# Performance work log

Measured on AMD Instinct MI355X. Metric: run time of the kernel, lower is better.

Reference implementation:

```python
import jax, jax.numpy as jnp
import numpy as np

DIM = 2048
N_HEADS = 16
HEAD_DIM = DIM // N_HEADS
ROPE_DIMS = 16
SEQ_LEN = 512
BATCH = 16


def _rope_cache(T):
    # freqs: [T, rd/2]
    inv = 1.0 / (10000.0 ** (jnp.arange(0, ROPE_DIMS, 2, dtype=jnp.float32) / ROPE_DIMS))
    t = jnp.arange(T, dtype=jnp.float32)
    freqs = jnp.outer(t, inv)
    return jnp.cos(freqs), jnp.sin(freqs)


def _apply_rope(x, cos, sin):
    # x: [B, H, T, hd]; rotate first ROPE_DIMS dims (half-split style)
    rd = ROPE_DIMS
    x_rope, x_pass = x[..., :rd], x[..., rd:]
    x1, x2 = x_rope[..., : rd // 2], x_rope[..., rd // 2:]
    c = cos[None, None, :, :]
    s = sin[None, None, :, :]
    rot = jnp.concatenate([x1 * c - x2 * s, x2 * c + x1 * s], axis=-1)
    return jnp.concatenate([rot, x_pass], axis=-1)


def setup_inputs() -> dict:
    key = jax.random.key(0)
    k1, k2, k3 = jax.random.split(key, 3)
    x = jax.random.normal(k1, (BATCH, SEQ_LEN, DIM), dtype=jnp.float32)
    Wqkv = jax.random.normal(k2, (DIM, 3 * DIM), dtype=jnp.float32) * (1.0 / np.sqrt(DIM))
    Wout = jax.random.normal(k3, (DIM, DIM), dtype=jnp.float32) * (1.0 / np.sqrt(DIM))
    return {"x": x, "Wqkv": Wqkv, "Wout": Wout}


def reference(x, Wqkv, Wout):
    B, T, C = x.shape
    H, hd = N_HEADS, HEAD_DIM
    qkv = (x @ Wqkv).reshape(B, T, 3, H, hd)
    q, k, v = qkv[:, :, 0], qkv[:, :, 1], qkv[:, :, 2]  # [B, T, H, hd]
    q = jnp.transpose(q, (0, 2, 1, 3))  # [B, H, T, hd]
    k = jnp.transpose(k, (0, 2, 1, 3))
    v = jnp.transpose(v, (0, 2, 1, 3))
    cos, sin = _rope_cache(T)
    q = _apply_rope(q, cos, sin)
    k = _apply_rope(k, cos, sin)
    scale = 1.0 / np.sqrt(hd)
    scores = jnp.einsum('bhqd,bhkd->bhqk', q, k) * scale
    causal = jnp.tril(jnp.ones((T, T), dtype=bool))
    scores = jnp.where(causal[None, None], scores, jnp.finfo(scores.dtype).min)
    attn = jax.nn.softmax(scores, axis=-1)
    y = jnp.einsum('bhqk,bhkd->bhqd', attn, v)  # [B, H, T, hd]
    y = jnp.transpose(y, (0, 2, 1, 3)).reshape(B, T, C)
    return y @ Wout
```

## Files before the change

kernel.cpp:

```cpp
#include <hip/hip_runtime.h>
#include <hip/hip_bf16.h>
#include <math.h>

using bf16 = __hip_bfloat16;
typedef short s16x8 __attribute__((ext_vector_type(8)));
typedef short s16x4 __attribute__((ext_vector_type(4)));
typedef float f32x4 __attribute__((ext_vector_type(4)));

#define DIM_C   2048
#define NHEADS  16
#define HEADD   128
#define SEQT    512
#define NBATCH  16
#define MROWS   (NBATCH*SEQT)
#define QKVN    (3*DIM_C)

static __device__ __forceinline__ float bf2f(bf16 v){ return __bfloat162float(v); }

static __device__ __forceinline__ void gl16(const void* g, void* l){
    __builtin_amdgcn_global_load_lds(
        reinterpret_cast<__attribute__((address_space(1))) void*>(
            (unsigned long long)g),
        reinterpret_cast<__attribute__((address_space(3))) void*>(
            (unsigned long long)l),
        16, 0, 0);
}

__global__ void k_cvt(const float* __restrict__ in, bf16* __restrict__ out, int n){
    size_t i = ((size_t)blockIdx.x*blockDim.x + threadIdx.x)*8;
    if (i >= (size_t)n) return;
    float4 a = *(const float4*)(in+i);
    float4 b = *(const float4*)(in+i+4);
    union { bf16 o[8]; s16x8 v; } u;
    u.o[0]=__float2bfloat16(a.x); u.o[1]=__float2bfloat16(a.y);
    u.o[2]=__float2bfloat16(a.z); u.o[3]=__float2bfloat16(a.w);
    u.o[4]=__float2bfloat16(b.x); u.o[5]=__float2bfloat16(b.y);
    u.o[6]=__float2bfloat16(b.z); u.o[7]=__float2bfloat16(b.w);
    *(s16x8*)(out+i) = u.v;
}

__global__ void k_transpose_cvt(const float* __restrict__ in, bf16* __restrict__ out,
                                int R, int C){
    __shared__ float tile[32][33];
    int c0 = blockIdx.x*32, r0 = blockIdx.y*32;
    int tx = threadIdx.x, ty = threadIdx.y;
    #pragma unroll
    for(int i=0;i<4;i++)
        tile[ty+8*i][tx] = in[(size_t)(r0+ty+8*i)*C + c0+tx];
    __syncthreads();
    #pragma unroll
    for(int i=0;i<4;i++)
        out[(size_t)(c0+ty+8*i)*R + r0+tx] = __float2bfloat16(tile[tx][ty+8*i]);
}

__global__ void k_vtrans(const bf16* __restrict__ qkv, bf16* __restrict__ vt){
    __shared__ bf16 tile[32][33];
    int t0 = blockIdx.x*32, d0 = blockIdx.y*32, bh = blockIdx.z;
    int b = bh>>4, h = bh&15;
    int tx = threadIdx.x, ty = threadIdx.y;
    const bf16* src = qkv + ((size_t)b*SEQT)*QKVN + 2*DIM_C + (size_t)h*HEADD;
    #pragma unroll
    for(int i=0;i<4;i++)
        tile[ty+8*i][tx] = src[(size_t)(t0+ty+8*i)*QKVN + d0+tx];
    __syncthreads();
    bf16* dst = vt + ((size_t)bh*HEADD)*SEQT;
    #pragma unroll
    for(int i=0;i<4;i++)
        dst[(size_t)(d0+ty+8*i)*SEQT + t0+tx] = tile[tx][ty+8*i];
}

__global__ void k_rope(bf16* __restrict__ qkv){
    int tid = blockIdx.x*blockDim.x + threadIdx.x;
    int i   = tid & 7;        int rest = tid >> 3;
    int qk  = rest & 1;       rest >>= 1;
    int h   = rest & 15;      rest >>= 4;
    int t   = rest & 511;     int b = rest >> 9;
    size_t base = ((size_t)(b*SEQT + t))*QKVN + (size_t)qk*DIM_C + (size_t)h*HEADD;
    float x1 = bf2f(qkv[base+i]), x2 = bf2f(qkv[base+i+8]);
    float inv = powf(10000.f, -(float)i/8.f);
    float fr = (float)t * inv;
    float c = cosf(fr), s = sinf(fr);
    qkv[base+i]   = __float2bfloat16(x1*c - x2*s);
    qkv[base+i+8] = __float2bfloat16(x2*c + x1*s);
}

static __device__ __forceinline__ void store_c(bf16* p, float v){ *p = __float2bfloat16(v); }
static __device__ __forceinline__ void store_c(float* p, float v){ *p = v; }

#define BAR()   __builtin_amdgcn_s_barrier()
#define SCHED() __builtin_amdgcn_sched_barrier(0)
#define LGKM0() asm volatile("s_waitcnt lgkmcnt(0)" ::: "memory")
#define VM6()   asm volatile("s_waitcnt vmcnt(6)"   ::: "memory")
#define VM0()   asm volatile("s_waitcnt vmcnt(0)"   ::: "memory")

template<typename OutT>
__global__ __launch_bounds__(512, 2) void k_gemm256(const bf16* __restrict__ A,
                                                    const bf16* __restrict__ Bt,
                                                    OutT* __restrict__ C,
                                                    int M, int N, int K){
    __shared__ __align__(16) bf16 As[2][2][128*64];
    __shared__ __align__(16) bf16 Bs[2][2][128*64];
    const int tid = threadIdx.x;
    const int wave = tid>>6, lane = tid&63, quad = lane>>4, l16 = lane&15;
    const int wm = wave>>2, wn = wave&3;

    const int nbx = gridDim.x;
    const int nwg = gridDim.x*gridDim.y;
    int bid = blockIdx.y*nbx + blockIdx.x;
    int swz = (bid&7)*(nwg>>3) + (bid>>3);
    int by = swz / nbx, bx = swz - by*nbx;
    const size_t rowbase = (size_t)by * 256;
    const size_t colbase = (size_t)bx * 256;
    const int NT = K>>6;

    f32x4 acc[8][4];
    #pragma unroll
    for(int i=0;i<8;i++)
        #pragma unroll
        for(int j=0;j<4;j++) acc[i][j] = (f32x4)(0.f);

    auto stageA = [&](int kt, int mh, bf16* dst){
        #pragma unroll
        for(int i=0;i<2;i++){
            int cb = i*512 + wave*64;
            int cc = cb + lane;
            int ri = cc>>3;
            int g  = (cc&7) ^ (ri&7);
            size_t grow = rowbase + (size_t)((ri>>6)<<7) + (mh<<6) + (ri&63);
            gl16(A + grow*(size_t)K + kt + g*8, dst + cb*8);
        }
    };
    auto stageB = [&](int kt, int nh, bf16* dst){
        #pragma unroll
        for(int i=0;i<2;i++){
            int cb = i*512 + wave*64;
            int cc = cb + lane;
            int ri = cc>>3;
            int g  = (cc&7) ^ (ri&7);
            size_t grow = colbase + (size_t)((ri>>5)<<6) + (nh<<5) + (ri&31);
            gl16(Bt + grow*(size_t)K + kt + g*8, dst + cb*8);
        }
    };
    auto ldsA = [&](int buf, int mh, int mi, int kc)->s16x8{
        int ri = wm*64 + mi*16 + l16;
        return *(const s16x8*)(&As[buf][mh][ri*64 + (((kc*4+quad) ^ (ri&7))<<3)]);
    };
    auto ldsB = [&](int buf, int nh, int nj, int kc)->s16x8{
        int ri = wn*32 + nj*16 + l16;
        return *(const s16x8*)(&Bs[buf][nh][ri*64 + (((kc*4+quad) ^ (ri&7))<<3)]);
    };

    s16x8 af[4][2], bf0[2][2], bf1[2][2];

#define MFMA16(MH,NH,BFR)                                                        \
    do{ _Pragma("unroll")                                                        \
        for(int mi_=0;mi_<4;mi_++){ _Pragma("unroll")                            \
            for(int nj_=0;nj_<2;nj_++){ _Pragma("unroll")                        \
                for(int kc_=0;kc_<2;kc_++)                                       \
                    acc[(MH)*4+mi_][(NH)*2+nj_] =                                \
                        __builtin_amdgcn_mfma_f32_16x16x32_bf16(                 \
                            af[mi_][kc_], BFR[nj_][kc_],                         \
                            acc[(MH)*4+mi_][(NH)*2+nj_], 0,0,0); } } }while(0)

    stageA(0, 0, &As[0][0][0]);
    stageB(0, 0, &Bs[0][0][0]);
    stageB(0, 1, &Bs[0][1][0]);
    stageA(0, 1, &As[0][1][0]);
    stageA(64, 0, &As[1][0][0]);
    stageB(64, 0, &Bs[1][0][0]);
    stageB(64, 1, &Bs[1][1][0]);
    VM6();
    BAR(); SCHED();

    for(int g=0; g<NT; ++g){
        const int cur = g&1, nxt = cur^1;
        const int kt1 = (g+1)<<6, kt2 = (g+2)<<6;
        #pragma unroll
        for(int mi=0;mi<4;mi++){ af[mi][0]=ldsA(cur,0,mi,0); af[mi][1]=ldsA(cur,0,mi,1); }
        #pragma unroll
        for(int nj=0;nj<2;nj++){ bf0[nj][0]=ldsB(cur,0,nj,0); bf0[nj][1]=ldsB(cur,0,nj,1); }
        if (g+1 < NT) stageA(kt1, 1, &As[nxt][1][0]);
        BAR(); LGKM0(); SCHED();
        __builtin_amdgcn_s_setprio(1);
        MFMA16(0,0,bf0);
        __builtin_amdgcn_s_setprio(0);
        BAR(); SCHED();
        #pragma unroll
        for(int nj=0;nj<2;nj++){ bf1[nj][0]=ldsB(cur,1,nj,0); bf1[nj][1]=ldsB(cur,1,nj,1); }
        if (g+2 < NT) stageA(kt2, 0, &As[cur][0][0]);
        BAR(); LGKM0(); SCHED();
        __builtin_amdgcn_s_setprio(1);
        MFMA16(0,1,bf1);
        __builtin_amdgcn_s_setprio(0);
        BAR(); SCHED();
        #pragma unroll
        for(int mi=0;mi<4;mi++){ af[mi][0]=ldsA(cur,1,mi,0); af[mi][1]=ldsA(cur,1,mi,1); }
        if (g+2 < NT) stageB(kt2, 0, &Bs[cur][0][0]);
        BAR(); LGKM0(); SCHED();
        __builtin_amdgcn_s_setprio(1);
        MFMA16(1,0,bf0);
        __builtin_amdgcn_s_setprio(0);
        BAR(); SCHED();
        if (g+2 < NT){ stageB(kt2, 1, &Bs[cur][1][0]); VM6(); } else { VM0(); }
        BAR(); SCHED();
        __builtin_amdgcn_s_setprio(1);
        MFMA16(1,1,bf1);
        __builtin_amdgcn_s_setprio(0);
        BAR(); SCHED();
    }
#undef MFMA16

    #pragma unroll
    for(int mf=0;mf<8;mf++)
        #pragma unroll
        for(int nf=0;nf<4;nf++)
            #pragma unroll
            for(int r=0;r<4;r++){
                size_t row = rowbase + wm*128 + mf*16 + quad*4 + r;
                size_t col = colbase + wn*64  + nf*16 + l16;
                store_c(C + row*(size_t)N + col, acc[mf][nf][r]);
            }
}

__global__ __launch_bounds__(256, 4) void k_attn(const bf16* __restrict__ qkv,
                                                 const bf16* __restrict__ vt,
                                                 bf16* __restrict__ y){
    __shared__ __align__(16) bf16 Ks[64*128];
    __shared__ __align__(16) bf16 Vs[128*64];
    __shared__ __align__(16) bf16 Ps[64*64];
    const int id = blockIdx.x;
    const int x  = id & 7, g = id >> 3;
    const int qt = 7 - (g >> 5);
    const int bh = ((g & 31) << 3) | x;
    const int b = bh >> 4, h = bh & 15;
    const int tid = threadIdx.x, wave = tid>>6, lane = tid&63, quad = lane>>4, l16 = lane&15;
    const int qbase = qt*64;
    const size_t rs = QKVN;
    const bf16* Qg = qkv + ((size_t)b*SEQT)*rs + (size_t)h*HEADD;
    const bf16* Kg = Qg + DIM_C;
    const bf16* Vtbh = vt + ((size_t)bh*HEADD)*SEQT;

    s16x8 qf[4];
    const int qrow = qbase + wave*16 + l16;
    {
        #pragma unroll
        for(int kc=0;kc<4;kc++)
            qf[kc] = *(const s16x8*)(Qg + (size_t)qrow*rs + kc*32 + quad*8);
    }
    f32x4 acc_o[8];
    #pragma unroll
    for(int dt=0;dt<8;dt++) acc_o[dt] = (f32x4)(0.f);
    float lsum = 0.f;
    const float C2 = 0.12751745f;
    const int nkt = qt + 1;

    for(int kt=0; kt<nkt; kt++){
        const int kbase = kt*64;
        const bool diag = (kt == nkt-1);
        __syncthreads();
        #pragma unroll
        for(int i=0;i<4;i++){
            int base = wave*256 + i*64;
            int cc   = base + lane;
            int rk   = cc>>4, gk = (cc&15) ^ (rk&7);
            gl16(Kg + (size_t)(kbase+rk)*rs + gk*8, &Ks[base*8]);
            int rv   = cc>>3, gv = (cc&7) ^ (rv&7);
            gl16(Vtbh + (size_t)rv*SEQT + kbase + gv*8, &Vs[base*8]);
        }
        __syncthreads();
        f32x4 sacc[4];
        #pragma unroll
        for(int ni=0;ni<4;ni++) sacc[ni] = (f32x4)(0.f);
        #pragma unroll
        for(int kc=0;kc<4;kc++){
            const int ch = kc*4 + quad;
            #pragma unroll
            for(int ni=0;ni<4;ni++){
                int r = ni*16 + l16;
                s16x8 kf = *(const s16x8*)(&Ks[r*128 + ((ch ^ (r&7))*8)]);
                sacc[ni] = __builtin_amdgcn_mfma_f32_16x16x32_bf16(kf, qf[kc], sacc[ni], 0,0,0);
            }
        }
        {
            const int row = wave*16 + l16;
            const int r7  = row & 7;
            #pragma unroll
            for(int ni=0;ni<4;ni++){
                union { s16x4 v; bf16 hh[4]; } pk;
                #pragma unroll
                for(int rr=0;rr<4;rr++){
                    float e = exp2f(sacc[ni][rr]*C2);
                    if (diag){ int kcol = kbase + ni*16 + quad*4 + rr; if (kcol > qrow) e = 0.f; }
                    lsum += e;
                    pk.hh[rr] = __float2bfloat16(e);
                }
                int c = ni*2 + (quad>>1);
                *(s16x4*)(&Ps[row*64 + ((c ^ r7)<<3) + ((quad&1)<<2)]) = pk.v;
            }
        }
        #pragma unroll
        for(int kk=0;kk<2;kk++){
            int rw = wave*16 + l16;
            int c  = kk*4 + quad;
            s16x8 pf = *(const s16x8*)(&Ps[rw*64 + ((c ^ (rw&7))<<3)]);
            #pragma unroll
            for(int dt=0;dt<8;dt++){
                int r = dt*16 + l16;
                s16x8 vf = *(const s16x8*)(&Vs[r*64 + ((c ^ (r&7))<<3)]);
                acc_o[dt] = __builtin_amdgcn_mfma_f32_16x16x32_bf16(vf, pf, acc_o[dt], 0,0,0);
            }
        }
    }
    lsum += __shfl_xor(lsum, 16, 64);
    lsum += __shfl_xor(lsum, 32, 64);
    float inv_l = 1.f/lsum;
    size_t base = ((size_t)(b*SEQT) + qrow)*DIM_C + (size_t)h*HEADD;
    #pragma unroll
    for(int dt=0;dt<8;dt++){
        union { s16x4 v; bf16 hh[4]; } o;
        #pragma unroll
        for(int rr=0;rr<4;rr++) o.hh[rr] = __float2bfloat16(acc_o[dt][rr]*inv_l);
        *(s16x4*)(y + base + dt*16 + quad*4) = o.v;
    }
}

extern "C" void kernel_launch(void* const* d_in, const int* in_sizes, int n_in,
                              void* d_out, int out_size, void* d_ws, size_t ws_size,
                              hipStream_t stream){
    const float* x    = (const float*)d_in[0];
    const float* Wqkv = (const float*)d_in[1];
    const float* Wout = (const float*)d_in[2];
    float* out = (float*)d_out;
    char* ws = (char*)d_ws;
    bf16* xb    = (bf16*)(ws + 0);
    bf16* vt    = (bf16*)(ws + 0);
    bf16* wqkvT = (bf16*)(ws + 33554432);
    bf16* woutT = (bf16*)(ws + 58720256);
    bf16* qkv   = (bf16*)(ws + 67108864);
    bf16* yb    = (bf16*)(ws + 167772160);

    k_cvt<<<dim3(MROWS*DIM_C/8/256), 256, 0, stream>>>(x, xb, MROWS*DIM_C);
    dim3 tb(32,8);
    k_transpose_cvt<<<dim3(QKVN/32, DIM_C/32), tb, 0, stream>>>(Wqkv, wqkvT, DIM_C, QKVN);
    k_transpose_cvt<<<dim3(DIM_C/32, DIM_C/32), tb, 0, stream>>>(Wout, woutT, DIM_C, DIM_C);

    k_gemm256<bf16><<<dim3(QKVN/256, MROWS/256), 512, 0, stream>>>(xb, wqkvT, qkv, MROWS, QKVN, DIM_C);
    k_rope<<<dim3(NBATCH*SEQT*NHEADS*2*8/256), 256, 0, stream>>>(qkv);
    k_vtrans<<<dim3(SEQT/32, HEADD/32, NBATCH*NHEADS), tb, 0, stream>>>(qkv, vt);
    k_attn<<<dim3(SEQT/64 * NHEADS * NBATCH), 256, 0, stream>>>(qkv, vt, yb);
    k_gemm256<float><<<dim3(DIM_C/256, MROWS/256), 512, 0, stream>>>(yb, woutT, out, MROWS, DIM_C, DIM_C);
}
```

Measured before the change: 509.1 us.

## Prefetch LDS fragments ahead of MFMA blocks in the GEMM main loop

Restructures the 256-tile GEMM loop so LDS fragment reads for the next MFMA block (and for the next k-tile) are issued before or during the current MFMA group, instead of being read and then fully waited on with lgkmcnt(0). This hides LDS latency behind matrix work. The MFMA loop order is also changed to kc-outer. The explicit lgkmcnt waits are removed and the compiler is left to insert the dependency waits. This risks more register pressure and relies on barrier placement to keep the double-buffered LDS reads correct.

```diff
diff --git a/kernel.cpp b/kernel.cpp
--- a/kernel.cpp
+++ b/kernel.cpp
@@ -89,7 +89,6 @@
 
 #define BAR()   __builtin_amdgcn_s_barrier()
 #define SCHED() __builtin_amdgcn_sched_barrier(0)
-#define LGKM0() asm volatile("s_waitcnt lgkmcnt(0)" ::: "memory")
 #define VM6()   asm volatile("s_waitcnt vmcnt(6)"   ::: "memory")
 #define VM0()   asm volatile("s_waitcnt vmcnt(0)"   ::: "memory")
 
@@ -152,11 +151,30 @@
 
     s16x8 af[4][2], bf0[2][2], bf1[2][2];
 
+    auto readA = [&](int buf, int mh){
+        #pragma unroll
+        for(int kc=0;kc<2;kc++)
+            #pragma unroll
+            for(int mi=0;mi<4;mi++) af[mi][kc] = ldsA(buf, mh, mi, kc);
+    };
+    auto readB0 = [&](int buf){
+        #pragma unroll
+        for(int kc=0;kc<2;kc++)
+            #pragma unroll
+            for(int nj=0;nj<2;nj++) bf0[nj][kc] = ldsB(buf, 0, nj, kc);
+    };
+    auto readB1 = [&](int buf){
+        #pragma unroll
+        for(int kc=0;kc<2;kc++)
+            #pragma unroll
+            for(int nj=0;nj<2;nj++) bf1[nj][kc] = ldsB(buf, 1, nj, kc);
+    };
+
 #define MFMA16(MH,NH,BFR)                                                        \
     do{ _Pragma("unroll")                                                        \
-        for(int mi_=0;mi_<4;mi_++){ _Pragma("unroll")                            \
-            for(int nj_=0;nj_<2;nj_++){ _Pragma("unroll")                        \
-                for(int kc_=0;kc_<2;kc_++)                                       \
+        for(int kc_=0;kc_<2;kc_++){ _Pragma("unroll")                            \
+            for(int mi_=0;mi_<4;mi_++){ _Pragma("unroll")                        \
+                for(int nj_=0;nj_<2;nj_++)                                       \
                     acc[(MH)*4+mi_][(NH)*2+nj_] =                                \
                         __builtin_amdgcn_mfma_f32_16x16x32_bf16(                 \
                             af[mi_][kc_], BFR[nj_][kc_],                         \
@@ -171,42 +189,41 @@
     stageB(64, 1, &Bs[1][1][0]);
     VM6();
     BAR(); SCHED();
+    readB0(0);
+    readA(0, 0);
 
     for(int g=0; g<NT; ++g){
         const int cur = g&1, nxt = cur^1;
         const int kt1 = (g+1)<<6, kt2 = (g+2)<<6;
-        #pragma unroll
-        for(int mi=0;mi<4;mi++){ af[mi][0]=ldsA(cur,0,mi,0); af[mi][1]=ldsA(cur,0,mi,1); }
-        #pragma unroll
-        for(int nj=0;nj<2;nj++){ bf0[nj][0]=ldsB(cur,0,nj,0); bf0[nj][1]=ldsB(cur,0,nj,1); }
+        readB1(cur);
         if (g+1 < NT) stageA(kt1, 1, &As[nxt][1][0]);
-        BAR(); LGKM0(); SCHED();
+        SCHED(); BAR(); SCHED();
         __builtin_amdgcn_s_setprio(1);
         MFMA16(0,0,bf0);
         __builtin_amdgcn_s_setprio(0);
-        BAR(); SCHED();
-        #pragma unroll
-        for(int nj=0;nj<2;nj++){ bf1[nj][0]=ldsB(cur,1,nj,0); bf1[nj][1]=ldsB(cur,1,nj,1); }
+        SCHED(); BAR();
         if (g+2 < NT) stageA(kt2, 0, &As[cur][0][0]);
-        BAR(); LGKM0(); SCHED();
+        SCHED(); BAR(); SCHED();
         __builtin_amdgcn_s_setprio(1);
         MFMA16(0,1,bf1);
         __builtin_amdgcn_s_setprio(0);
-        BAR(); SCHED();
-        #pragma unroll
-        for(int mi=0;mi<4;mi++){ af[mi][0]=ldsA(cur,1,mi,0); af[mi][1]=ldsA(cur,1,mi,1); }
+        readA(cur, 1);
+        SCHED(); BAR();
         if (g+2 < NT) stageB(kt2, 0, &Bs[cur][0][0]);
-        BAR(); LGKM0(); SCHED();
+        SCHED(); BAR(); SCHED();
         __builtin_amdgcn_s_setprio(1);
         MFMA16(1,0,bf0);
         __builtin_amdgcn_s_setprio(0);
-        BAR(); SCHED();
+        SCHED(); BAR();
         if (g+2 < NT){ stageB(kt2, 1, &Bs[cur][1][0]); VM6(); } else { VM0(); }
-        BAR(); SCHED();
+        SCHED(); BAR(); SCHED();
+        if (g+1 < NT) readB0(nxt);
+        SCHED();
         __builtin_amdgcn_s_setprio(1);
         MFMA16(1,1,bf1);
         __builtin_amdgcn_s_setprio(0);
-        BAR(); SCHED();
+        if (g+1 < NT) readA(nxt, 0);
+        SCHED(); BAR();
     }
 #undef MFMA16
 
```

After: 507.7 us. No clear change (-0.3%).

## Load A fragments directly from global to registers, stage only B via LDS

Applied to the files above, without the earlier changes.

The GEMM stops staging the A tile through shared memory and has each wave load its A fragments straight from global memory into registers. Only B goes through the double-buffered LDS pipeline, and the wait counts and barrier schedule are reworked around the new loads. This halves LDS use and removes the A LDS writes and reads, which could raise occupancy and cut LDS traffic. In exchange, the A loads are issued per wave without cross-wave reuse and their global latency sits close to the MFMAs, so stalls become more likely.

```diff
diff --git a/kernel.cpp b/kernel.cpp
--- a/kernel.cpp
+++ b/kernel.cpp
@@ -89,8 +89,7 @@
 
 #define BAR()   __builtin_amdgcn_s_barrier()
 #define SCHED() __builtin_amdgcn_sched_barrier(0)
-#define LGKM0() asm volatile("s_waitcnt lgkmcnt(0)" ::: "memory")
-#define VM6()   asm volatile("s_waitcnt vmcnt(6)"   ::: "memory")
+#define VM4()   asm volatile("s_waitcnt vmcnt(4)"   ::: "memory")
 #define VM0()   asm volatile("s_waitcnt vmcnt(0)"   ::: "memory")
 
 template<typename OutT>
@@ -98,7 +97,6 @@
                                                     const bf16* __restrict__ Bt,
                                                     OutT* __restrict__ C,
                                                     int M, int N, int K){
-    __shared__ __align__(16) bf16 As[2][2][128*64];
     __shared__ __align__(16) bf16 Bs[2][2][128*64];
     const int tid = threadIdx.x;
     const int wave = tid>>6, lane = tid&63, quad = lane>>4, l16 = lane&15;
@@ -119,17 +117,6 @@
         #pragma unroll
         for(int j=0;j<4;j++) acc[i][j] = (f32x4)(0.f);
 
-    auto stageA = [&](int kt, int mh, bf16* dst){
-        #pragma unroll
-        for(int i=0;i<2;i++){
-            int cb = i*512 + wave*64;
-            int cc = cb + lane;
-            int ri = cc>>3;
-            int g  = (cc&7) ^ (ri&7);
-            size_t grow = rowbase + (size_t)((ri>>6)<<7) + (mh<<6) + (ri&63);
-            gl16(A + grow*(size_t)K + kt + g*8, dst + cb*8);
-        }
-    };
     auto stageB = [&](int kt, int nh, bf16* dst){
         #pragma unroll
         for(int i=0;i<2;i++){
@@ -141,74 +128,83 @@
             gl16(Bt + grow*(size_t)K + kt + g*8, dst + cb*8);
         }
     };
-    auto ldsA = [&](int buf, int mh, int mi, int kc)->s16x8{
-        int ri = wm*64 + mi*16 + l16;
-        return *(const s16x8*)(&As[buf][mh][ri*64 + (((kc*4+quad) ^ (ri&7))<<3)]);
-    };
     auto ldsB = [&](int buf, int nh, int nj, int kc)->s16x8{
         int ri = wn*32 + nj*16 + l16;
         return *(const s16x8*)(&Bs[buf][nh][ri*64 + (((kc*4+quad) ^ (ri&7))<<3)]);
     };
 
+    const bf16* aRow[4];
+    #pragma unroll
+    for(int mi=0;mi<4;mi++)
+        aRow[mi] = A + (rowbase + (size_t)(wm*128 + mi*16 + l16))*(size_t)K + quad*8;
+    const size_t mhK = (size_t)64*(size_t)K;
+
     s16x8 af[4][2], bf0[2][2], bf1[2][2];
 
-#define MFMA16(MH,NH,BFR)                                                        \
-    do{ _Pragma("unroll")                                                        \
+#define LOAD_A(MH, KT) do{ _Pragma("unroll")                                     \
+    for(int mi_=0;mi_<4;mi_++){ _Pragma("unroll")                                \
+        for(int kc_=0;kc_<2;kc_++)                                               \
+            af[mi_][kc_] = *(const s16x8*)(aRow[mi_] + ((MH)?mhK:0)              \
+                                           + (size_t)(KT) + kc_*32); } }while(0)
+#define READ_B0(buf) do{ _Pragma("unroll")                                       \
+    for(int kc_=0;kc_<2;kc_++){ _Pragma("unroll")                                \
+        for(int nj_=0;nj_<2;nj_++) bf0[nj_][kc_] = ldsB((buf),0,nj_,kc_); } }while(0)
+#define READ_B1(buf) do{ _Pragma("unroll")                                       \
+    for(int kc_=0;kc_<2;kc_++){ _Pragma("unroll")                                \
+        for(int nj_=0;nj_<2;nj_++) bf1[nj_][kc_] = ldsB((buf),1,nj_,kc_); } }while(0)
+#define MFMA16(BFR, MH, NH) do{ _Pragma("unroll")                                \
+    for(int kc_=0;kc_<2;kc_++){ _Pragma("unroll")                                \
         for(int mi_=0;mi_<4;mi_++){ _Pragma("unroll")                            \
-            for(int nj_=0;nj_<2;nj_++){ _Pragma("unroll")                        \
-                for(int kc_=0;kc_<2;kc_++)                                       \
-                    acc[(MH)*4+mi_][(NH)*2+nj_] =                                \
-                        __builtin_amdgcn_mfma_f32_16x16x32_bf16(                 \
-                            af[mi_][kc_], BFR[nj_][kc_],                         \
-                            acc[(MH)*4+mi_][(NH)*2+nj_], 0,0,0); } } }while(0)
-
-    stageA(0, 0, &As[0][0][0]);
-    stageB(0, 0, &Bs[0][0][0]);
-    stageB(0, 1, &Bs[0][1][0]);
-    stageA(0, 1, &As[0][1][0]);
-    stageA(64, 0, &As[1][0][0]);
+            for(int nj_=0;nj_<2;nj_++)                                           \
+                acc[(MH)*4+mi_][(NH)*2+nj_] =                                    \
+                    __builtin_amdgcn_mfma_f32_16x16x32_bf16(                     \
+                        af[mi_][kc_], BFR[nj_][kc_],                             \
+                        acc[(MH)*4+mi_][(NH)*2+nj_], 0,0,0); } } }while(0)
+
+    stageB(0,  0, &Bs[0][0][0]);
+    stageB(0,  1, &Bs[0][1][0]);
     stageB(64, 0, &Bs[1][0][0]);
     stageB(64, 1, &Bs[1][1][0]);
-    VM6();
+    VM4();
     BAR(); SCHED();
+    READ_B0(0); READ_B1(0);
+    LOAD_A(0, 0);
 
     for(int g=0; g<NT; ++g){
         const int cur = g&1, nxt = cur^1;
         const int kt1 = (g+1)<<6, kt2 = (g+2)<<6;
-        #pragma unroll
-        for(int mi=0;mi<4;mi++){ af[mi][0]=ldsA(cur,0,mi,0); af[mi][1]=ldsA(cur,0,mi,1); }
-        #pragma unroll
-        for(int nj=0;nj<2;nj++){ bf0[nj][0]=ldsB(cur,0,nj,0); bf0[nj][1]=ldsB(cur,0,nj,1); }
-        if (g+1 < NT) stageA(kt1, 1, &As[nxt][1][0]);
-        BAR(); LGKM0(); SCHED();
-        __builtin_amdgcn_s_setprio(1);
-        MFMA16(0,0,bf0);
-        __builtin_amdgcn_s_setprio(0);
-        BAR(); SCHED();
-        #pragma unroll
-        for(int nj=0;nj<2;nj++){ bf1[nj][0]=ldsB(cur,1,nj,0); bf1[nj][1]=ldsB(cur,1,nj,1); }
-        if (g+2 < NT) stageA(kt2, 0, &As[cur][0][0]);
-        BAR(); LGKM0(); SCHED();
-        __builtin_amdgcn_s_setprio(1);
-        MFMA16(0,1,bf1);
-        __builtin_amdgcn_s_setprio(0);
-        BAR(); SCHED();
-        #pragma unroll
-        for(int mi=0;mi<4;mi++){ af[mi][0]=ldsA(cur,1,mi,0); af[mi][1]=ldsA(cur,1,mi,1); }
-        if (g+2 < NT) stageB(kt2, 0, &Bs[cur][0][0]);
-        BAR(); LGKM0(); SCHED();
-        __builtin_amdgcn_s_setprio(1);
-        MFMA16(1,0,bf0);
-        __builtin_amdgcn_s_setprio(0);
-        BAR(); SCHED();
-        if (g+2 < NT){ stageB(kt2, 1, &Bs[cur][1][0]); VM6(); } else { VM0(); }
         BAR(); SCHED();
         __builtin_amdgcn_s_setprio(1);
-        MFMA16(1,1,bf1);
+        MFMA16(bf0, 0,0);
         __builtin_amdgcn_s_setprio(0);
+        if (g+2 < NT) stageB(kt2, 0, &Bs[cur][0][0]);
+        SCHED();
         BAR(); SCHED();
+        __builtin_amdgcn_s_setprio(1);
+        MFMA16(bf1, 0,1);
+        __builtin_amdgcn_s_setprio(0);
+        if (g+2 < NT) VM4(); else VM0();
+        SCHED();
+        LOAD_A(1, (g<<6));
+        SCHED();
+        BAR(); SCHED();
+        __builtin_amdgcn_s_setprio(1);
+        MFMA16(bf0, 1,0);
+        __builtin_amdgcn_s_setprio(0);
+        if (g+1 < NT) READ_B0(nxt);
+        if (g+2 < NT){ stageB(kt2, 1, &Bs[cur][1][0]); VM4(); } else { VM0(); }
+        SCHED();
+        BAR(); SCHED();
+        __builtin_amdgcn_s_setprio(1);
+        MFMA16(bf1, 1,1);
+        __builtin_amdgcn_s_setprio(0);
+        if (g+1 < NT){ READ_B1(nxt); LOAD_A(0, kt1); }
+        SCHED();
     }
 #undef MFMA16
+#undef READ_B1
+#undef READ_B0
+#undef LOAD_A
 
     #pragma unroll
     for(int mf=0;mf<8;mf++)
```

New measurement: 889.6 us. +74.7%, slower.
